# Kernel optimization log

Measured on AMD Instinct MI355X. Metric: run time of the kernel, lower is better.

The kernel has to match this reference:

```python
import jax, jax.numpy as jnp
import numpy as np


def _layernorm(x, g, b, eps=1e-5):
    mu = jnp.mean(x, axis=-1, keepdims=True)
    var = jnp.mean((x - mu) ** 2, axis=-1, keepdims=True)
    return g * (x - mu) * jax.lax.rsqrt(var + eps) + b


def _pos_encoding(S, D, dtype):
    # standard sinusoidal positional encoding [S, D]
    pos = jnp.arange(S, dtype=jnp.float32)[:, None]
    i = jnp.arange(0, D, 2, dtype=jnp.float32)[None, :]
    ang = pos / jnp.power(10000.0, i / D)
    return jnp.stack([jnp.sin(ang), jnp.cos(ang)], axis=-1).reshape(S, D).astype(dtype)


def _mha(x, theta, Wc, bc, num_heads):
    # Quantum projection: per-wire RX(x)+RX(theta) from |0>, <Z> = cos(x+theta).
    # The module uses ONE shared q_layer for q, k, v, so q == k == v.
    B, S, D = x.shape
    dk = D // num_heads
    p = jnp.cos(x + theta)                                    # [B,S,D]
    ph = p.reshape(B, S, num_heads, dk)                        # [B,S,H,dk]
    scale = 1.0 / jnp.sqrt(jnp.asarray(dk, x.dtype))
    scores = jnp.einsum('bqhd,bkhd->bhqk', ph, ph) * scale     # [B,H,S,S]
    attn = jax.nn.softmax(scores, axis=-1)
    out = jnp.einsum('bhqk,bkhd->bqhd', attn, ph).reshape(B, S, D)
    return out @ Wc + bc


def _ffn(x, theta, W1, b1, W2, b2):
    # RY-encoder + trainable RY per wire -> <Z> = cos(x + theta)
    h = jnp.cos(x + theta)
    h = h @ W1 + b1
    return jax.nn.relu(h) @ W2 + b2


def _forward(tokens, embedding, theta_attn, Wc, bc, ln1_g, ln1_b, theta_ffn,
             W1, b1, W2, b2, ln2_g, ln2_b, Wcls, bcls, num_heads):
    x = embedding[tokens]                                      # [B,S,D]
    B, S, D = x.shape
    x = x + _pos_encoding(S, D, x.dtype)
    n_blocks = theta_attn.shape[0]
    for l in range(n_blocks):  # small fixed layer count
        a = _mha(x, theta_attn[l], Wc[l], bc[l], num_heads)
        x = _layernorm(x + a, ln1_g[l], ln1_b[l])
        f = _ffn(x, theta_ffn[l], W1[l], b1[l], W2[l], b2[l])
        x = _layernorm(x + f, ln2_g[l], ln2_b[l])
    pooled = jnp.mean(x, axis=1)                               # [B,D]
    return pooled @ Wcls + bcls                                # [B,C]


def setup_inputs() -> dict:
    key = jax.random.key(0)
    ks = jax.random.split(key, 8)
    V, D, L, F, C = 32000, 512, 2, 2048, 10
    B, S = 8, 1024
    s = 0.02
    return {
        'tokens': jax.random.randint(ks[0], (B, S), 0, V, dtype=jnp.int32),
        'embedding': jax.random.normal(ks[1], (V, D), jnp.float32) * s,
        'theta_attn': jax.random.normal(ks[2], (L, D), jnp.float32) * s,
        'Wc': jax.random.normal(ks[3], (L, D, D), jnp.float32) * s,
        'bc': jnp.zeros((L, D), jnp.float32),
        'ln1_g': jnp.ones((L, D), jnp.float32),
        'ln1_b': jnp.zeros((L, D), jnp.float32),
        'theta_ffn': jax.random.normal(ks[4], (L, D), jnp.float32) * s,
        'W1': jax.random.normal(ks[5], (L, D, F), jnp.float32) * s,
        'b1': jnp.zeros((L, F), jnp.float32),
        'W2': jax.random.normal(ks[6], (L, F, D), jnp.float32) * s,
        'b2': jnp.zeros((L, D), jnp.float32),
        'ln2_g': jnp.ones((L, D), jnp.float32),
        'ln2_b': jnp.zeros((L, D), jnp.float32),
        'Wcls': jax.random.normal(ks[7], (D, C), jnp.float32) * s,
        'bcls': jnp.zeros((C,), jnp.float32),
        'num_heads': 8,
    }


def reference(tokens, embedding, theta_attn, Wc, bc, ln1_g, ln1_b, theta_ffn,
              W1, b1, W2, b2, ln2_g, ln2_b, Wcls, bcls, num_heads):
    return _forward(tokens, embedding, theta_attn, Wc, bc, ln1_g, ln1_b,
                    theta_ffn, W1, b1, W2, b2, ln2_g, ln2_b, Wcls, bcls, num_heads)
```

## Files before the change

kernel.cpp:

```cpp
#include <hip/hip_runtime.h>
#include <math.h>

#define BB 8
#define SS 1024
#define DD 512
#define HH 8
#define DK 64
#define FF 2048
#define NCLS 10
#define ROWS (BB*SS)
#define NLAYERS 2

typedef short bf16x8 __attribute__((ext_vector_type(8)));
typedef float f32x4 __attribute__((ext_vector_type(4)));

__device__ inline short f2bf(float f) {
    unsigned u = __float_as_uint(f);
    u += 0x7FFF + ((u >> 16) & 1);
    return (short)(u >> 16);
}

__device__ inline void gload_lds16(const void* g, void* l) {
    __builtin_amdgcn_global_load_lds((const __attribute__((address_space(1))) void*)g,
                                     (__attribute__((address_space(3))) void*)l, 16, 0, 0);
}

__global__ __launch_bounds__(128) void k_embed_pe(const int* __restrict__ tokens,
                                                  const float* __restrict__ emb,
                                                  float* __restrict__ x) {
    int row = blockIdx.x;
    int s = row & (SS - 1);
    int tok = tokens[row];
    const float4* e = reinterpret_cast<const float4*>(emb + (size_t)tok * DD);
    float4 v = e[threadIdx.x];
    float pe[4];
#pragma unroll
    for (int j = 0; j < 4; ++j) {
        int d = threadIdx.x * 4 + j;
        int jj = d >> 1;
        float inv = expf(-((float)(2 * jj) / (float)DD) * 9.210340371976184f);
        float ang = (float)s * inv;
        pe[j] = (d & 1) ? cosf(ang) : sinf(ang);
    }
    v.x += pe[0]; v.y += pe[1]; v.z += pe[2]; v.w += pe[3];
    reinterpret_cast<float4*>(x + (size_t)row * DD)[threadIdx.x] = v;
}

template <int WT>
__global__ __launch_bounds__(256) void k_cosp(const float* __restrict__ x,
                                              const float* __restrict__ theta,
                                              short* __restrict__ p,
                                              short* __restrict__ pt) {
    int d0 = blockIdx.x * 64, s0 = blockIdx.y * 64, b = blockIdx.z;
    int t = threadIdx.x;
    int tc = t & 15, tr = t >> 4;
    __shared__ short lt[64][68];
    float4 th = *reinterpret_cast<const float4*>(theta + d0 + tc * 4);
#pragma unroll
    for (int i = 0; i < 4; ++i) {
        int s = tr + 16 * i;
        float4 xv = *reinterpret_cast<const float4*>(
            x + ((size_t)b * SS + s0 + s) * DD + d0 + tc * 4);
        short4 o;
        o.x = f2bf(cosf(xv.x + th.x));
        o.y = f2bf(cosf(xv.y + th.y));
        o.z = f2bf(cosf(xv.z + th.z));
        o.w = f2bf(cosf(xv.w + th.w));
        *reinterpret_cast<short4*>(p + ((size_t)b * SS + s0 + s) * DD + d0 + tc * 4) = o;
        if (WT) {
            lt[tc * 4 + 0][s] = o.x;
            lt[tc * 4 + 1][s] = o.y;
            lt[tc * 4 + 2][s] = o.z;
            lt[tc * 4 + 3][s] = o.w;
        }
    }
    if (WT) {
        __syncthreads();
#pragma unroll
        for (int i = 0; i < 4; ++i) {
            int d = tr + 16 * i;
            short4 v;
            v.x = lt[d][tc * 4 + 0];
            v.y = lt[d][tc * 4 + 1];
            v.z = lt[d][tc * 4 + 2];
            v.w = lt[d][tc * 4 + 3];
            *reinterpret_cast<short4*>(pt + ((size_t)b * DD + d0 + d) * SS + s0 + tc * 4) = v;
        }
    }
}

__global__ __launch_bounds__(256) void k_wtrans(const float* __restrict__ W,
                                                short* __restrict__ Wt,
                                                int K, int N) {
    __shared__ float tile[32][33];
    int n0 = blockIdx.x * 32, k0 = blockIdx.y * 32;
    int tx = threadIdx.x & 31, ty = threadIdx.x >> 5;
#pragma unroll
    for (int i = 0; i < 4; ++i)
        tile[ty + 8 * i][tx] = W[(size_t)(k0 + ty + 8 * i) * N + n0 + tx];
    __syncthreads();
#pragma unroll
    for (int i = 0; i < 4; ++i)
        Wt[(size_t)(n0 + ty + 8 * i) * K + k0 + tx] = f2bf(tile[tx][ty + 8 * i]);
}

__global__ __launch_bounds__(256) void k_attn(const short* __restrict__ p,
                                              const short* __restrict__ pt,
                                              short* __restrict__ aout) {
    int qc = blockIdx.x, h = blockIdx.y, b = blockIdx.z;
    int t = threadIdx.x, w = t >> 6, l = t & 63;
    int lg = l >> 4, lr = l & 15;

    __shared__ __attribute__((aligned(16))) short Kt[128 * 64];
    __shared__ __attribute__((aligned(16))) short Vt[64 * 128];
    __shared__ __attribute__((aligned(16))) short Pl[4][16 * 136];

    const size_t prow = ((size_t)b * SS + qc * 64 + w * 16 + lr) * DD + h * DK;
    bf16x8 qf0 = *reinterpret_cast<const bf16x8*>(p + prow + lg * 8);
    bf16x8 qf1 = *reinterpret_cast<const bf16x8*>(p + prow + 32 + lg * 8);

    f32x4 acc[4];
#pragma unroll
    for (int dt = 0; dt < 4; ++dt) acc[dt] = (f32x4){0.f, 0.f, 0.f, 0.f};
    float denom = 0.f;

    const short* pK = p + (size_t)b * SS * DD + h * DK;
    const short* pV = pt + ((size_t)b * DD + h * DK) * SS;

    short* myP = &Pl[w][0];

    for (int k0 = 0; k0 < SS; k0 += 128) {
        __syncthreads();
#pragma unroll
        for (int i = 0; i < 4; ++i) {
            int c = i * 256 + t;
            int row = c >> 3, sl = c & 7, ssl = sl ^ (row & 7);
            gload_lds16(pK + (size_t)(k0 + row) * DD + ssl * 8,
                        Kt + (size_t)(i * 256 + w * 64) * 8);
        }
#pragma unroll
        for (int i = 0; i < 4; ++i) {
            int c = i * 256 + t;
            int row = c >> 4, sl = c & 15, ssl = sl ^ ((row & 7) * 2);
            gload_lds16(pV + (size_t)row * SS + k0 + ssl * 8,
                        Vt + (size_t)(i * 256 + w * 64) * 8);
        }
        asm volatile("s_waitcnt vmcnt(0)" ::: "memory");
        __syncthreads();

        f32x4 sc[8];
#pragma unroll
        for (int kt = 0; kt < 8; ++kt) {
            int row = kt * 16 + lr;
            bf16x8 ka0 = *reinterpret_cast<const bf16x8*>(Kt + row * 64 + ((lg ^ (row & 7)) * 8));
            bf16x8 ka1 = *reinterpret_cast<const bf16x8*>(Kt + row * 64 + (((lg + 4) ^ (row & 7)) * 8));
            f32x4 z = (f32x4){0.f, 0.f, 0.f, 0.f};
            z = __builtin_amdgcn_mfma_f32_16x16x32_bf16(ka0, qf0, z, 0, 0, 0);
            z = __builtin_amdgcn_mfma_f32_16x16x32_bf16(ka1, qf1, z, 0, 0, 0);
            sc[kt] = z;
        }
#pragma unroll
        for (int kt = 0; kt < 8; ++kt) {
            float e0 = __expf(sc[kt].x * 0.125f);
            float e1 = __expf(sc[kt].y * 0.125f);
            float e2 = __expf(sc[kt].z * 0.125f);
            float e3 = __expf(sc[kt].w * 0.125f);
            denom += (e0 + e1) + (e2 + e3);
            short4 pk;
            pk.x = f2bf(e0); pk.y = f2bf(e1); pk.z = f2bf(e2); pk.w = f2bf(e3);
            *reinterpret_cast<short4*>(myP + lr * 136 + kt * 16 + lg * 4) = pk;
        }
        asm volatile("s_waitcnt lgkmcnt(0)" ::: "memory");
#pragma unroll
        for (int kt2 = 0; kt2 < 4; ++kt2) {
            bf16x8 pb = *reinterpret_cast<const bf16x8*>(myP + lr * 136 + kt2 * 32 + lg * 8);
#pragma unroll
            for (int dt = 0; dt < 4; ++dt) {
                int row = dt * 16 + lr;
                bf16x8 va = *reinterpret_cast<const bf16x8*>(
                    Vt + row * 128 + (((kt2 * 4 + lg) ^ ((row & 7) * 2)) * 8));
                acc[dt] = __builtin_amdgcn_mfma_f32_16x16x32_bf16(va, pb, acc[dt], 0, 0, 0);
            }
        }
    }

    denom += __shfl_xor(denom, 16);
    denom += __shfl_xor(denom, 32);
    float inv = 1.0f / denom;

    size_t orow = ((size_t)b * SS + qc * 64 + w * 16 + lr) * DD + h * DK;
#pragma unroll
    for (int dt = 0; dt < 4; ++dt) {
        short4 o;
        o.x = f2bf(acc[dt].x * inv);
        o.y = f2bf(acc[dt].y * inv);
        o.z = f2bf(acc[dt].z * inv);
        o.w = f2bf(acc[dt].w * inv);
        *reinterpret_cast<short4*>(aout + orow + dt * 16 + lg * 4) = o;
    }
}

template <int RELU, int OUTBF>
__global__ __launch_bounds__(256) void k_mm(const short* __restrict__ A,
                                            const short* __restrict__ Bt,
                                            const float* __restrict__ bias,
                                            void* __restrict__ C,
                                            int N, int K, int gx) {
    __shared__ __attribute__((aligned(16))) short Al[4][128 * 32];
    __shared__ __attribute__((aligned(16))) short Bl[4][128 * 32];
    int t = threadIdx.x, w = t >> 6, l = t & 63;
    int lg = l >> 4, lr = l & 15;
    int wm = w >> 1, wn = w & 1;

    int nwg = gridDim.x;
    int bid = blockIdx.x;
    int swz = (bid & 7) * (nwg >> 3) + (bid >> 3);
    int bx = swz % gx, by = swz / gx;
    int row0 = by * 128, col0 = bx * 128;

    f32x4 acc[4][4];
#pragma unroll
    for (int m = 0; m < 4; ++m)
#pragma unroll
        for (int n = 0; n < 4; ++n) acc[m][n] = (f32x4){0.f, 0.f, 0.f, 0.f};

#define STAGE_MM(buf, kk0)                                                      \
    {                                                                           \
        _Pragma("unroll")                                                       \
        for (int i = 0; i < 2; ++i) {                                           \
            int c = i * 256 + t;                                                \
            int row = c >> 2, sl = c & 3, ssl = sl ^ ((row >> 1) & 3);          \
            gload_lds16(A + (size_t)(row0 + row) * K + (kk0) + ssl * 8,         \
                        &Al[buf][0] + (size_t)(i * 256 + w * 64) * 8);          \
            gload_lds16(Bt + (size_t)(col0 + row) * K + (kk0) + ssl * 8,        \
                        &Bl[buf][0] + (size_t)(i * 256 + w * 64) * 8);          \
        }                                                                       \
    }

    const int nk = K >> 5;
    STAGE_MM(0, 0);
    if (nk > 1) STAGE_MM(1, 32);
    if (nk > 2) STAGE_MM(2, 64);

    for (int kt = 0; kt < nk; ++kt) {
        if (kt + 2 < nk)
            asm volatile("s_waitcnt vmcnt(8)\n\ts_barrier" ::: "memory");
        else if (kt + 1 < nk)
            asm volatile("s_waitcnt vmcnt(4)\n\ts_barrier" ::: "memory");
        else
            asm volatile("s_waitcnt vmcnt(0)\n\ts_barrier" ::: "memory");

        const short* a_ = &Al[kt & 3][0];
        const short* b_ = &Bl[kt & 3][0];
        bf16x8 af[4], bfr[4];
#pragma unroll
        for (int m = 0; m < 4; ++m) {
            int row = wm * 64 + m * 16 + lr;
            af[m] = *reinterpret_cast<const bf16x8*>(a_ + row * 32 + ((lg ^ ((row >> 1) & 3)) * 8));
        }
#pragma unroll
        for (int n = 0; n < 4; ++n) {
            int row = wn * 64 + n * 16 + lr;
            bfr[n] = *reinterpret_cast<const bf16x8*>(b_ + row * 32 + ((lg ^ ((row >> 1) & 3)) * 8));
        }
        if (kt + 3 < nk) STAGE_MM((kt + 3) & 3, (kt + 3) * 32);

#pragma unroll
        for (int m = 0; m < 4; ++m)
#pragma unroll
            for (int n = 0; n < 4; ++n)
                acc[m][n] = __builtin_amdgcn_mfma_f32_16x16x32_bf16(af[m], bfr[n], acc[m][n], 0, 0, 0);
    }
#undef STAGE_MM

    float bv[4];
#pragma unroll
    for (int n = 0; n < 4; ++n) bv[n] = bias[col0 + wn * 64 + n * 16 + lr];

#pragma unroll
    for (int m = 0; m < 4; ++m) {
#pragma unroll
        for (int n = 0; n < 4; ++n) {
            int col = col0 + wn * 64 + n * 16 + lr;
#pragma unroll
            for (int j = 0; j < 4; ++j) {
                int row = row0 + wm * 64 + m * 16 + lg * 4 + j;
                float v = acc[m][n][j] + bv[n];
                if (RELU) v = fmaxf(v, 0.f);
                if (OUTBF) ((short*)C)[(size_t)row * N + col] = f2bf(v);
                else       ((float*)C)[(size_t)row * N + col] = v;
            }
        }
    }
}

template <int COSP>
__global__ __launch_bounds__(128) void k_add_ln(float* __restrict__ x,
                                                const float* __restrict__ rr,
                                                const float* __restrict__ g,
                                                const float* __restrict__ bb,
                                                const float* __restrict__ theta,
                                                short* __restrict__ p) {
    int row = blockIdx.x;
    int t = threadIdx.x;
    float4 v = *reinterpret_cast<const float4*>(x + (size_t)row * DD + t * 4);
    float4 av = *reinterpret_cast<const float4*>(rr + (size_t)row * DD + t * 4);
    v.x += av.x; v.y += av.y; v.z += av.z; v.w += av.w;
    float s = v.x + v.y + v.z + v.w;
    float s2 = v.x * v.x + v.y * v.y + v.z * v.z + v.w * v.w;
#pragma unroll
    for (int off = 32; off > 0; off >>= 1) {
        s += __shfl_down(s, off);
        s2 += __shfl_down(s2, off);
    }
    __shared__ float ls[2], ls2[2];
    if ((t & 63) == 0) { ls[t >> 6] = s; ls2[t >> 6] = s2; }
    __syncthreads();
    float S1 = ls[0] + ls[1];
    float S2 = ls2[0] + ls2[1];
    float mu = S1 * (1.0f / DD);
    float var = S2 * (1.0f / DD) - mu * mu;
    float rstd = rsqrtf(var + 1e-5f);
    float4 gv = *reinterpret_cast<const float4*>(g + t * 4);
    float4 bv = *reinterpret_cast<const float4*>(bb + t * 4);
    float4 o;
    o.x = gv.x * (v.x - mu) * rstd + bv.x;
    o.y = gv.y * (v.y - mu) * rstd + bv.y;
    o.z = gv.z * (v.z - mu) * rstd + bv.z;
    o.w = gv.w * (v.w - mu) * rstd + bv.w;
    *reinterpret_cast<float4*>(x + (size_t)row * DD + t * 4) = o;
    if (COSP) {
        float4 th = *reinterpret_cast<const float4*>(theta + t * 4);
        short4 pk;
        pk.x = f2bf(cosf(o.x + th.x));
        pk.y = f2bf(cosf(o.y + th.y));
        pk.z = f2bf(cosf(o.z + th.z));
        pk.w = f2bf(cosf(o.w + th.w));
        *reinterpret_cast<short4*>(p + (size_t)row * DD + t * 4) = pk;
    }
}

__global__ __launch_bounds__(128) void k_pool(const float* __restrict__ x,
                                              float* __restrict__ part) {
    int b = blockIdx.x, c = blockIdx.y;
    int t = threadIdx.x;
    float4 s = {0.f, 0.f, 0.f, 0.f};
    for (int i = 0; i < 32; ++i) {
        float4 v = reinterpret_cast<const float4*>(
            x + ((size_t)b * SS + c * 32 + i) * DD)[t];
        s.x += v.x; s.y += v.y; s.z += v.z; s.w += v.w;
    }
    reinterpret_cast<float4*>(part + ((size_t)b * 32 + c) * DD)[t] = s;
}

__global__ __launch_bounds__(512) void k_cls(const float* __restrict__ part,
                                             const float* __restrict__ Wcls,
                                             const float* __restrict__ bcls,
                                             float* __restrict__ out) {
    int b = blockIdx.x;
    int t = threadIdx.x;
    float s = 0.f;
    for (int i = 0; i < 32; ++i) s += part[((size_t)b * 32 + i) * DD + t];
    float pooled = s * (1.0f / SS);
    float acc[NCLS];
#pragma unroll
    for (int c = 0; c < NCLS; ++c) acc[c] = pooled * Wcls[t * NCLS + c];
#pragma unroll
    for (int off = 32; off > 0; off >>= 1)
#pragma unroll
        for (int c = 0; c < NCLS; ++c) acc[c] += __shfl_xor(acc[c], off);
    __shared__ float wp[8][NCLS];
    int w = t >> 6, l = t & 63;
    if (l == 0)
#pragma unroll
        for (int c = 0; c < NCLS; ++c) wp[w][c] = acc[c];
    __syncthreads();
    if (t < NCLS) {
        float o = bcls[t];
#pragma unroll
        for (int i = 0; i < 8; ++i) o += wp[i][t];
        out[b * NCLS + t] = o;
    }
}

extern "C" void kernel_launch(void* const* d_in, const int* in_sizes, int n_in,
                              void* d_out, int out_size, void* d_ws, size_t ws_size,
                              hipStream_t stream) {
    const int* tokens      = (const int*)d_in[0];
    const float* emb       = (const float*)d_in[1];
    const float* theta_att = (const float*)d_in[2];
    const float* Wc        = (const float*)d_in[3];
    const float* bc        = (const float*)d_in[4];
    const float* ln1_g     = (const float*)d_in[5];
    const float* ln1_b     = (const float*)d_in[6];
    const float* theta_ffn = (const float*)d_in[7];
    const float* W1        = (const float*)d_in[8];
    const float* b1        = (const float*)d_in[9];
    const float* W2        = (const float*)d_in[10];
    const float* b2        = (const float*)d_in[11];
    const float* ln2_g     = (const float*)d_in[12];
    const float* ln2_b     = (const float*)d_in[13];
    const float* Wcls      = (const float*)d_in[14];
    const float* bcls      = (const float*)d_in[15];
    float* out = (float*)d_out;

    char* wsb = (char*)d_ws;
    float* x    = (float*)(wsb);
    float* t0   = (float*)(wsb + (size_t)16 * 1048576);
    short* p    = (short*)(wsb + (size_t)32 * 1048576);
    short* pt   = (short*)(wsb + (size_t)40 * 1048576);
    short* a    = (short*)(wsb + (size_t)48 * 1048576);
    short* hh   = (short*)(wsb + (size_t)56 * 1048576);
    short* Wct  = (short*)(wsb + (size_t)88 * 1048576);
    short* W1t  = (short*)(wsb + (size_t)89 * 1048576);
    short* W2t  = (short*)(wsb + (size_t)91 * 1048576);
    float* part = (float*)(wsb + (size_t)94 * 1048576);

    k_embed_pe<<<ROWS, 128, 0, stream>>>(tokens, emb, x);

    for (int l = 0; l < NLAYERS; ++l) {
        k_wtrans<<<dim3(DD / 32, DD / 32), 256, 0, stream>>>(Wc + (size_t)l * DD * DD, Wct, DD, DD);
        k_wtrans<<<dim3(FF / 32, DD / 32), 256, 0, stream>>>(W1 + (size_t)l * DD * FF, W1t, DD, FF);
        k_wtrans<<<dim3(DD / 32, FF / 32), 256, 0, stream>>>(W2 + (size_t)l * FF * DD, W2t, FF, DD);

        k_cosp<1><<<dim3(DD / 64, SS / 64, BB), 256, 0, stream>>>(x, theta_att + l * DD, p, pt);
        k_attn<<<dim3(SS / 64, HH, BB), 256, 0, stream>>>(p, pt, a);
        k_mm<0, 0><<<(DD / 128) * (ROWS / 128), 256, 0, stream>>>(
            a, Wct, bc + l * DD, t0, DD, DD, DD / 128);
        k_add_ln<1><<<ROWS, 128, 0, stream>>>(x, t0, ln1_g + l * DD, ln1_b + l * DD,
                                              theta_ffn + l * DD, p);
        k_mm<1, 1><<<(FF / 128) * (ROWS / 128), 256, 0, stream>>>(
            p, W1t, b1 + l * FF, hh, FF, DD, FF / 128);
        k_mm<0, 0><<<(DD / 128) * (ROWS / 128), 256, 0, stream>>>(
            hh, W2t, b2 + l * DD, t0, DD, FF, DD / 128);
        k_add_ln<0><<<ROWS, 128, 0, stream>>>(x, t0, ln2_g + l * DD, ln2_b + l * DD,
                                              (const float*)nullptr, (short*)nullptr);
    }

    k_pool<<<dim3(BB, 32), 128, 0, stream>>>(x, part);
    k_cls<<<BB, 512, 0, stream>>>(part, Wcls, bcls, out);
}
```

Measured before the change: 426.8 us.

## Pipeline attention K/V loads with triple buffering and double the query rows per block

Restructures the attention kernel so each block handles 128 query rows, with each wave processing two 16-row slices against the same K/V tiles. K/V tiles shrink to 64 keys and are staged into a 3-deep LDS ring with asynchronous global-to-LDS loads issued two tiles ahead, replacing the load-wait-compute loop. The kernel also sets MFMA sections to higher wave priority and flattens the grid index so a query chunk's blocks cover all batch/head pairs. This is meant to hide global load latency and halve K/V traffic per query, at the cost of more registers, more LDS and fewer blocks (512 instead of 1024).

```diff
diff --git a/kernel.cpp b/kernel.cpp
--- a/kernel.cpp
+++ b/kernel.cpp
@@ -104,99 +104,126 @@
         Wt[(size_t)(n0 + ty + 8 * i) * K + k0 + tx] = f2bf(tile[tx][ty + 8 * i]);
 }
 
+#define KVB 64
+#define NT (SS / KVB)
 __global__ __launch_bounds__(256) void k_attn(const short* __restrict__ p,
                                               const short* __restrict__ pt,
                                               short* __restrict__ aout) {
-    int qc = blockIdx.x, h = blockIdx.y, b = blockIdx.z;
+    int bid = blockIdx.x;
+    int qc = bid >> 6, bh = bid & 63;
+    int b = bh >> 3, h = bh & 7;
     int t = threadIdx.x, w = t >> 6, l = t & 63;
     int lg = l >> 4, lr = l & 15;
 
-    __shared__ __attribute__((aligned(16))) short Kt[128 * 64];
-    __shared__ __attribute__((aligned(16))) short Vt[64 * 128];
-    __shared__ __attribute__((aligned(16))) short Pl[4][16 * 136];
-
-    const size_t prow = ((size_t)b * SS + qc * 64 + w * 16 + lr) * DD + h * DK;
-    bf16x8 qf0 = *reinterpret_cast<const bf16x8*>(p + prow + lg * 8);
-    bf16x8 qf1 = *reinterpret_cast<const bf16x8*>(p + prow + 32 + lg * 8);
-
-    f32x4 acc[4];
-#pragma unroll
-    for (int dt = 0; dt < 4; ++dt) acc[dt] = (f32x4){0.f, 0.f, 0.f, 0.f};
-    float denom = 0.f;
+    __shared__ __attribute__((aligned(16))) short Kt[3][KVB * 64];
+    __shared__ __attribute__((aligned(16))) short Vt[3][64 * KVB];
+    __shared__ __attribute__((aligned(16))) short Pl[4][16 * 72];
+
+    bf16x8 qf[2][2];
+#pragma unroll
+    for (int s = 0; s < 2; ++s) {
+        size_t prow = ((size_t)b * SS + qc * 128 + w * 32 + s * 16 + lr) * DD + h * DK;
+        qf[s][0] = *reinterpret_cast<const bf16x8*>(p + prow + lg * 8);
+        qf[s][1] = *reinterpret_cast<const bf16x8*>(p + prow + 32 + lg * 8);
+    }
+
+    f32x4 acc[2][4];
+#pragma unroll
+    for (int s = 0; s < 2; ++s)
+#pragma unroll
+        for (int dt = 0; dt < 4; ++dt) acc[s][dt] = (f32x4){0.f, 0.f, 0.f, 0.f};
+    float denom[2] = {0.f, 0.f};
 
     const short* pK = p + (size_t)b * SS * DD + h * DK;
     const short* pV = pt + ((size_t)b * DD + h * DK) * SS;
-
     short* myP = &Pl[w][0];
 
-    for (int k0 = 0; k0 < SS; k0 += 128) {
-        __syncthreads();
-#pragma unroll
-        for (int i = 0; i < 4; ++i) {
-            int c = i * 256 + t;
-            int row = c >> 3, sl = c & 7, ssl = sl ^ (row & 7);
-            gload_lds16(pK + (size_t)(k0 + row) * DD + ssl * 8,
-                        Kt + (size_t)(i * 256 + w * 64) * 8);
-        }
-#pragma unroll
-        for (int i = 0; i < 4; ++i) {
-            int c = i * 256 + t;
-            int row = c >> 4, sl = c & 15, ssl = sl ^ ((row & 7) * 2);
-            gload_lds16(pV + (size_t)row * SS + k0 + ssl * 8,
-                        Vt + (size_t)(i * 256 + w * 64) * 8);
-        }
-        asm volatile("s_waitcnt vmcnt(0)" ::: "memory");
-        __syncthreads();
-
-        f32x4 sc[8];
-#pragma unroll
-        for (int kt = 0; kt < 8; ++kt) {
-            int row = kt * 16 + lr;
-            bf16x8 ka0 = *reinterpret_cast<const bf16x8*>(Kt + row * 64 + ((lg ^ (row & 7)) * 8));
-            bf16x8 ka1 = *reinterpret_cast<const bf16x8*>(Kt + row * 64 + (((lg + 4) ^ (row & 7)) * 8));
-            f32x4 z = (f32x4){0.f, 0.f, 0.f, 0.f};
-            z = __builtin_amdgcn_mfma_f32_16x16x32_bf16(ka0, qf0, z, 0, 0, 0);
-            z = __builtin_amdgcn_mfma_f32_16x16x32_bf16(ka1, qf1, z, 0, 0, 0);
-            sc[kt] = z;
-        }
-#pragma unroll
-        for (int kt = 0; kt < 8; ++kt) {
-            float e0 = __expf(sc[kt].x * 0.125f);
-            float e1 = __expf(sc[kt].y * 0.125f);
-            float e2 = __expf(sc[kt].z * 0.125f);
-            float e3 = __expf(sc[kt].w * 0.125f);
-            denom += (e0 + e1) + (e2 + e3);
-            short4 pk;
-            pk.x = f2bf(e0); pk.y = f2bf(e1); pk.z = f2bf(e2); pk.w = f2bf(e3);
-            *reinterpret_cast<short4*>(myP + lr * 136 + kt * 16 + lg * 4) = pk;
-        }
-        asm volatile("s_waitcnt lgkmcnt(0)" ::: "memory");
-#pragma unroll
-        for (int kt2 = 0; kt2 < 4; ++kt2) {
-            bf16x8 pb = *reinterpret_cast<const bf16x8*>(myP + lr * 136 + kt2 * 32 + lg * 8);
-#pragma unroll
-            for (int dt = 0; dt < 4; ++dt) {
-                int row = dt * 16 + lr;
-                bf16x8 va = *reinterpret_cast<const bf16x8*>(
-                    Vt + row * 128 + (((kt2 * 4 + lg) ^ ((row & 7) * 2)) * 8));
-                acc[dt] = __builtin_amdgcn_mfma_f32_16x16x32_bf16(va, pb, acc[dt], 0, 0, 0);
+#define STAGE_ATT(bi, kk0)                                                      \
+    {                                                                           \
+        _Pragma("unroll")                                                       \
+        for (int i = 0; i < 2; ++i) {                                           \
+            int c = i * 256 + t;                                                \
+            int row = c >> 3, sl = c & 7, ssl = sl ^ (row & 7);                 \
+            gload_lds16(pK + (size_t)((kk0) + row) * DD + ssl * 8,              \
+                        &Kt[bi][0] + (size_t)(i * 256 + w * 64) * 8);           \
+            gload_lds16(pV + (size_t)row * SS + (kk0) + ssl * 8,                \
+                        &Vt[bi][0] + (size_t)(i * 256 + w * 64) * 8);           \
+        }                                                                       \
+    }
+
+    STAGE_ATT(0, 0);
+    STAGE_ATT(1, KVB);
+
+    for (int kt3 = 0; kt3 < NT; ++kt3) {
+        if (kt3 + 1 < NT)
+            asm volatile("s_waitcnt vmcnt(4)\n\ts_barrier" ::: "memory");
+        else
+            asm volatile("s_waitcnt vmcnt(0)\n\ts_barrier" ::: "memory");
+        if (kt3 + 2 < NT) STAGE_ATT((kt3 + 2) % 3, (kt3 + 2) * KVB);
+
+        const short* kb = &Kt[kt3 % 3][0];
+        const short* vb = &Vt[kt3 % 3][0];
+
+#pragma unroll
+        for (int s = 0; s < 2; ++s) {
+            f32x4 sc[4];
+            __builtin_amdgcn_s_setprio(1);
+#pragma unroll
+            for (int kt = 0; kt < 4; ++kt) {
+                int row = kt * 16 + lr;
+                bf16x8 ka0 = *reinterpret_cast<const bf16x8*>(kb + row * 64 + ((lg ^ (row & 7)) * 8));
+                bf16x8 ka1 = *reinterpret_cast<const bf16x8*>(kb + row * 64 + (((lg + 4) ^ (row & 7)) * 8));
+                f32x4 z = (f32x4){0.f, 0.f, 0.f, 0.f};
+                z = __builtin_amdgcn_mfma_f32_16x16x32_bf16(ka0, qf[s][0], z, 0, 0, 0);
+                z = __builtin_amdgcn_mfma_f32_16x16x32_bf16(ka1, qf[s][1], z, 0, 0, 0);
+                sc[kt] = z;
             }
-        }
-    }
-
-    denom += __shfl_xor(denom, 16);
-    denom += __shfl_xor(denom, 32);
-    float inv = 1.0f / denom;
-
-    size_t orow = ((size_t)b * SS + qc * 64 + w * 16 + lr) * DD + h * DK;
-#pragma unroll
-    for (int dt = 0; dt < 4; ++dt) {
-        short4 o;
-        o.x = f2bf(acc[dt].x * inv);
-        o.y = f2bf(acc[dt].y * inv);
-        o.z = f2bf(acc[dt].z * inv);
-        o.w = f2bf(acc[dt].w * inv);
-        *reinterpret_cast<short4*>(aout + orow + dt * 16 + lg * 4) = o;
+            __builtin_amdgcn_s_setprio(0);
+#pragma unroll
+            for (int kt = 0; kt < 4; ++kt) {
+                float e0 = __expf(sc[kt].x * 0.125f);
+                float e1 = __expf(sc[kt].y * 0.125f);
+                float e2 = __expf(sc[kt].z * 0.125f);
+                float e3 = __expf(sc[kt].w * 0.125f);
+                denom[s] += (e0 + e1) + (e2 + e3);
+                short4 pk;
+                pk.x = f2bf(e0); pk.y = f2bf(e1); pk.z = f2bf(e2); pk.w = f2bf(e3);
+                *reinterpret_cast<short4*>(myP + lr * 72 + kt * 16 + lg * 4) = pk;
+            }
+            asm volatile("s_waitcnt lgkmcnt(0)" ::: "memory");
+            __builtin_amdgcn_s_setprio(1);
+#pragma unroll
+            for (int kt2 = 0; kt2 < 2; ++kt2) {
+                bf16x8 pb = *reinterpret_cast<const bf16x8*>(myP + lr * 72 + kt2 * 32 + lg * 8);
+#pragma unroll
+                for (int dt = 0; dt < 4; ++dt) {
+                    int row = dt * 16 + lr;
+                    bf16x8 va = *reinterpret_cast<const bf16x8*>(
+                        vb + row * 64 + (((kt2 * 4 + lg) ^ (row & 7)) * 8));
+                    acc[s][dt] = __builtin_amdgcn_mfma_f32_16x16x32_bf16(va, pb, acc[s][dt], 0, 0, 0);
+                }
+            }
+            __builtin_amdgcn_s_setprio(0);
+        }
+    }
+#undef STAGE_ATT
+
+#pragma unroll
+    for (int s = 0; s < 2; ++s) {
+        float d2 = denom[s];
+        d2 += __shfl_xor(d2, 16);
+        d2 += __shfl_xor(d2, 32);
+        float inv = 1.0f / d2;
+        size_t orow = ((size_t)b * SS + qc * 128 + w * 32 + s * 16 + lr) * DD + h * DK;
+#pragma unroll
+        for (int dt = 0; dt < 4; ++dt) {
+            short4 o;
+            o.x = f2bf(acc[s][dt].x * inv);
+            o.y = f2bf(acc[s][dt].y * inv);
+            o.z = f2bf(acc[s][dt].z * inv);
+            o.w = f2bf(acc[s][dt].w * inv);
+            *reinterpret_cast<short4*>(aout + orow + dt * 16 + lg * 4) = o;
+        }
     }
 }
 
@@ -424,7 +451,7 @@
         k_wtrans<<<dim3(DD / 32, FF / 32), 256, 0, stream>>>(W2 + (size_t)l * FF * DD, W2t, FF, DD);
 
         k_cosp<1><<<dim3(DD / 64, SS / 64, BB), 256, 0, stream>>>(x, theta_att + l * DD, p, pt);
-        k_attn<<<dim3(SS / 64, HH, BB), 256, 0, stream>>>(p, pt, a);
+        k_attn<<<(SS / 128) * BB * HH, 256, 0, stream>>>(p, pt, a);
         k_mm<0, 0><<<(DD / 128) * (ROWS / 128), 256, 0, stream>>>(
             a, Wct, bc + l * DD, t0, DD, DD, DD / 128);
         k_add_ln<1><<<ROWS, 128, 0, stream>>>(x, t0, ln1_g + l * DD, ln1_b + l * DD,
```

Measured after the change: 418.8 us. No clear change (-1.9%).
